# Optimization experiments

Measured on AMD Instinct MI355X. Metric: run time of the kernel, lower is better.

The kernel has to match this reference:

```python
import jax, jax.numpy as jnp
import numpy as np

D = 512    # d_model == EMBED_DIM
H = 8      # nhead
FF = 2048  # dim_feedforward
T, B, S, M = 64, 32, 64, 256
EPS = 1e-5


def setup_inputs() -> dict:
    key = jax.random.key(0)
    ks = iter(jax.random.split(key, 40))
    rn = lambda k, shp, s=0.02: s * jax.random.normal(k, shp, jnp.float32)
    inp = {
        'tgt': jax.random.normal(next(ks), (T, B, D), jnp.float32),
        'memory': jax.random.normal(next(ks), (M, B, D), jnp.float32),
        'semantics': jax.random.normal(next(ks), (B, S, D), jnp.float32),
    }
    for pfx in ('pt', 'sa', 'ca'):  # pre_target, self_attn, cross multihead_attn
        inp[pfx + '_wqkv'] = rn(next(ks), (3 * D, D))
        inp[pfx + '_bqkv'] = jnp.zeros((3 * D,), jnp.float32)
        inp[pfx + '_wo'] = rn(next(ks), (D, D))
        inp[pfx + '_bo'] = jnp.zeros((D,), jnp.float32)
    # relevant_mlp_pre_target: fc0 (2D->D), relu, fc1 (D->D), relu, fc2 (D->1)
    inp['mlp_w0'] = rn(next(ks), (D, 2 * D), float(np.sqrt(2.0 / (2 * D))))
    inp['mlp_b0'] = jnp.zeros((D,), jnp.float32)
    inp['mlp_w1'] = rn(next(ks), (D, D), float(np.sqrt(2.0 / D)))
    inp['mlp_b1'] = jnp.zeros((D,), jnp.float32)
    inp['mlp_w2'] = rn(next(ks), (1, D), float(np.sqrt(2.0 / D)))
    inp['mlp_b2'] = jnp.zeros((1,), jnp.float32)
    inp['ffn_w1'] = rn(next(ks), (FF, D))
    inp['ffn_b1'] = jnp.zeros((FF,), jnp.float32)
    inp['ffn_w2'] = rn(next(ks), (D, FF))
    inp['ffn_b2'] = jnp.zeros((D,), jnp.float32)
    for i in (1, 2, 3):
        inp[f'ln{i}_g'] = jnp.ones((D,), jnp.float32)
        inp[f'ln{i}_b'] = jnp.zeros((D,), jnp.float32)
    return inp


def layernorm(x, g, b):
    mu = jnp.mean(x, -1, keepdims=True)
    var = jnp.var(x, -1, keepdims=True)
    return (x - mu) * jax.lax.rsqrt(var + EPS) * g + b


def mha(q, k, v, wqkv, bqkv, wo, bo):
    # q,k,v: (L, B, D) seq-first, like torch nn.MultiheadAttention
    hd = D // H
    wq, wk, wv = jnp.split(wqkv, 3, axis=0)
    bq, bk, bv = jnp.split(bqkv, 3)
    qh = (q @ wq.T + bq).reshape(q.shape[0], q.shape[1], H, hd)
    kh = (k @ wk.T + bk).reshape(k.shape[0], k.shape[1], H, hd)
    vh = (v @ wv.T + bv).reshape(v.shape[0], v.shape[1], H, hd)
    scale = 1.0 / float(np.sqrt(hd))
    att = jax.nn.softmax(jnp.einsum('qbhd,kbhd->bhqk', qh * scale, kh), axis=-1)
    out = jnp.einsum('bhqk,kbhd->qbhd', att, vh).reshape(q.shape[0], q.shape[1], D)
    return out @ wo.T + bo


def get_relevant_semantic(feats, sem, w0, b0, w1, b1, w2, b2):
    # feats: (B,T,D), sem: (B,S,D). Linear-on-concat == sum of two linears, so we
    # never materialize the (B,T,S,2D) cat tensor; hidden (B,T,S,D) is unavoidable math.
    w0c, w0s = w0[:, :D], w0[:, D:]
    h = (feats @ w0c.T)[:, :, None, :] + (sem @ w0s.T)[:, None, :, :] + b0  # (B,T,S,D)
    h = jax.nn.relu(h)
    h = jax.nn.relu(h @ w1.T + b1)
    scores = h @ w2.T + b2                      # (B,T,S,1)
    a = jax.nn.softmax(scores, axis=2)          # softmax over sem axis
    return jnp.sum(sem[:, None, :, :] * a, axis=2)  # (B,T,D)


def reference(tgt, memory, semantics,
              pt_wqkv, pt_bqkv, pt_wo, pt_bo,
              sa_wqkv, sa_bqkv, sa_wo, sa_bo,
              ca_wqkv, ca_bqkv, ca_wo, ca_bo,
              mlp_w0, mlp_b0, mlp_w1, mlp_b1, mlp_w2, mlp_b2,
              ffn_w1, ffn_b1, ffn_w2, ffn_b2,
              ln1_g, ln1_b, ln2_g, ln2_b, ln3_g, ln3_b):
    # MULTIHEAD_PRE_TARGET branch (eval mode: dropout = identity)
    rel = get_relevant_semantic(jnp.transpose(tgt, (1, 0, 2)), semantics,
                                mlp_w0, mlp_b0, mlp_w1, mlp_b1, mlp_w2, mlp_b2)
    sem_k = jnp.transpose(rel, (1, 0, 2))  # (T,B,D) seq-first key/value
    x = tgt + mha(tgt, sem_k, sem_k, pt_wqkv, pt_bqkv, pt_wo, pt_bo)
    # self attention
    x = layernorm(x + mha(x, x, x, sa_wqkv, sa_bqkv, sa_wo, sa_bo), ln1_g, ln1_b)
    # cross attention over encoder memory
    x = layernorm(x + mha(x, memory, memory, ca_wqkv, ca_bqkv, ca_wo, ca_bo), ln2_g, ln2_b)
    # feed-forward
    ff = jax.nn.relu(x @ ffn_w1.T + ffn_b1) @ ffn_w2.T + ffn_b2
    return layernorm(x + ff, ln3_g, ln3_b)
```

## Files before the change

### kernel.cpp

```cpp
#include <hip/hip_runtime.h>
#include <hip/hip_bf16.h>

#define WS_B 32
#define WS_T 64
#define WS_S 64
#define WS_D 512

typedef __attribute__((ext_vector_type(8))) __bf16 bf16x8;
typedef __attribute__((ext_vector_type(4))) float f32x4;
typedef unsigned short ushort_t;

#define MB(x) ((size_t)(x) << 20)

__device__ __forceinline__ unsigned packpair(float lo, float hi) {
    return ((__float_as_uint(lo) + 0x8000u) >> 16) |
           ((__float_as_uint(hi) + 0x8000u) & 0xffff0000u);
}
__device__ __forceinline__ ushort_t f2bf(float x) {
    return (ushort_t)((__float_as_uint(x) + 0x8000u) >> 16);
}
__device__ __forceinline__ float bf2f(ushort_t u) {
    return __uint_as_float(((unsigned)u) << 16);
}
__device__ __forceinline__ unsigned fuse_word(unsigned f, unsigned s) {
    float lo = __uint_as_float(f << 16) + __uint_as_float(s << 16);
    float hi = __uint_as_float(f & 0xffff0000u) + __uint_as_float(s & 0xffff0000u);
    lo = fmaxf(lo, 0.f);
    hi = fmaxf(hi, 0.f);
    return packpair(lo, hi);
}

struct CvtArgs {
    const float* src[13];
    ushort_t* dst[13];
    int n4[13];
};
__global__ __launch_bounds__(256) void megacvt_kernel(CvtArgs a) {
    const int t = blockIdx.y;
    const int n = a.n4[t];
    const float4* S = (const float4*)a.src[t];
    uint2* D = (uint2*)a.dst[t];
    for (int i = blockIdx.x * 256 + threadIdx.x; i < n; i += gridDim.x * 256) {
        float4 v = S[i];
        uint2 o;
        o.x = packpair(v.x, v.y);
        o.y = packpair(v.z, v.w);
        D[i] = o;
    }
}

__global__ __launch_bounds__(512, 2) void mfma_gemm(
    const ushort_t* __restrict__ A, int lda,
    const ushort_t* __restrict__ W, int ldw,
    const float* __restrict__ bias,
    const float* __restrict__ resid,
    float* __restrict__ C,
    ushort_t* __restrict__ Cb,
    int ldc, int K, int relu)
{
    __shared__ ushort_t As[128 * 32];
    __shared__ ushort_t Bs[256 * 32];
    const int tid = threadIdx.x;
    const int mb = blockIdx.y, nb = blockIdx.x;
    const int w = tid >> 6, lane = tid & 63;
    const int wm = w & 1, wn = w >> 1;
    const int l15 = lane & 15, quad = lane >> 4;
    const int arow = tid >> 2, akc = tid & 3;

    const ushort_t* Ap  = A + (long)(mb * 128 + arow) * lda + akc * 8;
    const ushort_t* Bp0 = W + (long)(nb * 256 + arow) * ldw + akc * 8;
    const ushort_t* Bp1 = Bp0 + (long)128 * ldw;
    ushort_t* Asw  = &As[arow * 32 + akc * 8];
    ushort_t* Bsw0 = &Bs[arow * 32 + akc * 8];
    ushort_t* Bsw1 = Bsw0 + 128 * 32;

    f32x4 acc[4][4];
#pragma unroll
    for (int i = 0; i < 4; ++i)
#pragma unroll
        for (int j = 0; j < 4; ++j) acc[i][j] = (f32x4)0.f;

    for (int k0 = 0; k0 < K; k0 += 32) {
        uint4 av  = *(const uint4*)(Ap + k0);
        uint4 bb0 = *(const uint4*)(Bp0 + k0);
        uint4 bb1 = *(const uint4*)(Bp1 + k0);
        __syncthreads();
        *(uint4*)Asw  = av;
        *(uint4*)Bsw0 = bb0;
        *(uint4*)Bsw1 = bb1;
        __syncthreads();
        bf16x8 af[4], bf[4];
#pragma unroll
        for (int mt = 0; mt < 4; ++mt)
            af[mt] = *(const bf16x8*)&As[(wm * 64 + mt * 16 + l15) * 32 + quad * 8];
#pragma unroll
        for (int nt = 0; nt < 4; ++nt)
            bf[nt] = *(const bf16x8*)&Bs[(wn * 64 + nt * 16 + l15) * 32 + quad * 8];
#pragma unroll
        for (int mt = 0; mt < 4; ++mt)
#pragma unroll
            for (int nt = 0; nt < 4; ++nt)
                acc[mt][nt] = __builtin_amdgcn_mfma_f32_16x16x32_bf16(
                    af[mt], bf[nt], acc[mt][nt], 0, 0, 0);
    }

#pragma unroll
    for (int nt = 0; nt < 4; ++nt) {
        const int col = nb * 256 + wn * 64 + nt * 16 + l15;
        const float bv = bias ? bias[col] : 0.f;
#pragma unroll
        for (int mt = 0; mt < 4; ++mt) {
            const int row0 = mb * 128 + wm * 64 + mt * 16 + quad * 4;
#pragma unroll
            for (int rg = 0; rg < 4; ++rg) {
                float v = acc[mt][nt][rg] + bv;
                if (relu) v = fmaxf(v, 0.f);
                const long off = (long)(row0 + rg) * ldc + col;
                if (resid) v += resid[off];
                if (C) C[off] = v;
                if (Cb) Cb[off] = f2bf(v);
            }
        }
    }
}

__global__ __launch_bounds__(512, 2) void h2score_kernel(
    const ushort_t* __restrict__ Fb,
    const ushort_t* __restrict__ Sb,
    const ushort_t* __restrict__ w1b,
    const float* __restrict__ b1,
    const float* __restrict__ w2,
    float* __restrict__ scores4)
{
    __shared__ ushort_t As[128 * 32];
    __shared__ ushort_t Bs[256 * 32];
    __shared__ float scred[128 * 4];
    const int tid = threadIdx.x;
    const int mb = blockIdx.x, nb = blockIdx.y;
    const int w = tid >> 6, lane = tid & 63;
    const int wm = w & 1, wn = w >> 1;
    const int l15 = lane & 15, quad = lane >> 4;

    const int arow = tid >> 2, akc = tid & 3;
    const int m_g = mb * 128 + arow;
    const int r = m_g >> 6, s = m_g & 63, bidx = r & 31;
    const ushort_t* Fp = Fb + (long)r * 512 + akc * 8;
    const ushort_t* Sp = Sb + (long)(bidx * 64 + s) * 512 + akc * 8;
    const ushort_t* Bp0 = w1b + (long)(nb * 256 + (tid >> 2)) * 512 + (tid & 3) * 8;
    const ushort_t* Bp1 = Bp0 + (long)128 * 512;
    ushort_t* Asw = &As[arow * 32 + akc * 8];
    ushort_t* Bsw0 = &Bs[(tid >> 2) * 32 + (tid & 3) * 8];
    ushort_t* Bsw1 = Bsw0 + 128 * 32;

    f32x4 acc[4][4];
#pragma unroll
    for (int i = 0; i < 4; ++i)
#pragma unroll
        for (int j = 0; j < 4; ++j) acc[i][j] = (f32x4)0.f;

    for (int k0 = 0; k0 < 512; k0 += 32) {
        uint4 fa = *(const uint4*)(Fp + k0);
        uint4 sa = *(const uint4*)(Sp + k0);
        uint4 bb0 = *(const uint4*)(Bp0 + k0);
        uint4 bb1 = *(const uint4*)(Bp1 + k0);
        __syncthreads();
        uint4 o;
        o.x = fuse_word(fa.x, sa.x);
        o.y = fuse_word(fa.y, sa.y);
        o.z = fuse_word(fa.z, sa.z);
        o.w = fuse_word(fa.w, sa.w);
        *(uint4*)Asw = o;
        *(uint4*)Bsw0 = bb0;
        *(uint4*)Bsw1 = bb1;
        __syncthreads();
        bf16x8 af[4], bf[4];
#pragma unroll
        for (int mt = 0; mt < 4; ++mt)
            af[mt] = *(const bf16x8*)&As[(wm * 64 + mt * 16 + l15) * 32 + quad * 8];
#pragma unroll
        for (int nt = 0; nt < 4; ++nt)
            bf[nt] = *(const bf16x8*)&Bs[(wn * 64 + nt * 16 + l15) * 32 + quad * 8];
#pragma unroll
        for (int mt = 0; mt < 4; ++mt)
#pragma unroll
            for (int nt = 0; nt < 4; ++nt)
                acc[mt][nt] = __builtin_amdgcn_mfma_f32_16x16x32_bf16(
                    af[mt], bf[nt], acc[mt][nt], 0, 0, 0);
    }
    __syncthreads();

    float sp[4][4];
#pragma unroll
    for (int mt = 0; mt < 4; ++mt)
#pragma unroll
        for (int rg = 0; rg < 4; ++rg) sp[mt][rg] = 0.f;
#pragma unroll
    for (int nt = 0; nt < 4; ++nt) {
        const int col = nb * 256 + wn * 64 + nt * 16 + l15;
        const float cb = b1[col];
        const float cw = w2[col];
#pragma unroll
        for (int mt = 0; mt < 4; ++mt) {
#pragma unroll
            for (int rg = 0; rg < 4; ++rg)
                sp[mt][rg] += fmaxf(acc[mt][nt][rg] + cb, 0.f) * cw;
        }
    }
#pragma unroll
    for (int mt = 0; mt < 4; ++mt)
#pragma unroll
        for (int rg = 0; rg < 4; ++rg) {
            float v = sp[mt][rg];
            v += __shfl_xor(v, 1);
            v += __shfl_xor(v, 2);
            v += __shfl_xor(v, 4);
            v += __shfl_xor(v, 8);
            if (l15 == 0)
                scred[(wm * 64 + mt * 16 + quad * 4 + rg) * 4 + wn] = v;
        }
    __syncthreads();
    if (tid < 128) {
        float t = scred[tid * 4] + scred[tid * 4 + 1]
                + scred[tid * 4 + 2] + scred[tid * 4 + 3];
        scores4[(long)nb * 131072 + mb * 128 + tid] = t;
    }
}

__global__ __launch_bounds__(256) void softrel_kernel(
    const float* __restrict__ sc4,
    const float* __restrict__ sem,
    ushort_t* __restrict__ rel)
{
    __shared__ float a_s[64];
    const int tid = threadIdx.x;
    const int r = blockIdx.x;
    const int b = r & (WS_B - 1);
    if (tid < 64) {
        float t = sc4[r * 64 + tid] + sc4[131072 + r * 64 + tid];
        float m = t;
#pragma unroll
        for (int off = 32; off > 0; off >>= 1) m = fmaxf(m, __shfl_xor(m, off));
        float e = __expf(t - m);
        float su = e;
#pragma unroll
        for (int off = 32; off > 0; off >>= 1) su += __shfl_xor(su, off);
        a_s[tid] = e / su;
    }
    __syncthreads();
#pragma unroll
    for (int dd = 0; dd < 2; ++dd) {
        const int d = tid + dd * 256;
        float accd = 0.f;
        const float* sp = sem + (long)b * 64 * 512 + d;
        for (int s = 0; s < 64; ++s)
            accd += a_s[s] * sp[s * 512];
        rel[(long)r * 512 + d] = f2bf(accd);
    }
}

__global__ __launch_bounds__(256) void attn2_kernel(
    const ushort_t* __restrict__ Qm, int ldq, int qoff,
    const ushort_t* __restrict__ Km, int ldk, int koff,
    const ushort_t* __restrict__ Vm, int ldv, int voff,
    ushort_t* __restrict__ O,
    int Lk)
{
    __shared__ float sQT[64 * 34];
    __shared__ float sKT[64 * 68];
    __shared__ float sS[32 * 260];
    __shared__ float sredm[8 * 34];
    __shared__ float sreds[8 * 34];
    const int tid = threadIdx.x;
    const int b  = blockIdx.x >> 4;
    const int h  = (blockIdx.x >> 1) & 7;
    const int qt = blockIdx.x & 1;
    const int L8 = Lk >> 3;

    {
        const int q = tid >> 3, c = tid & 7;
        const int qg = qt * 32 + q;
        const ushort_t* pp = Qm + (long)(qg * WS_B + b) * ldq + qoff + h * 64 + c * 8;
        uint4 u = *(const uint4*)pp;
        const ushort_t* us = (const ushort_t*)&u;
#pragma unroll
        for (int i = 0; i < 8; ++i)
            sQT[(c * 8 + i) * 34 + q] = bf2f(us[i]);
    }

    const int k4 = (tid & 15) * 4;
    const int q2 = (tid >> 4) * 2;

    for (int kt = 0; kt < Lk; kt += 64) {
        __syncthreads();
        {
            const int kk = tid >> 3, c = tid & 7;
#pragma unroll
            for (int half = 0; half < 2; ++half) {
                const int kr = kk + half * 32;
                const ushort_t* pp = Km + (long)((kt + kr) * WS_B + b) * ldk + koff + h * 64 + c * 8;
                uint4 u = *(const uint4*)pp;
                const ushort_t* us = (const ushort_t*)&u;
#pragma unroll
                for (int i = 0; i < 8; ++i)
                    sKT[(c * 8 + i) * 68 + kr] = bf2f(us[i]);
            }
        }
        __syncthreads();
        float acc[2][4] = {{0.f, 0.f, 0.f, 0.f}, {0.f, 0.f, 0.f, 0.f}};
        for (int d = 0; d < 64; ++d) {
            const float qa = sQT[d * 34 + q2];
            const float qb = sQT[d * 34 + q2 + 1];
            const float4 kv = *(const float4*)&sKT[d * 68 + k4];
            acc[0][0] += qa * kv.x; acc[0][1] += qa * kv.y;
            acc[0][2] += qa * kv.z; acc[0][3] += qa * kv.w;
            acc[1][0] += qb * kv.x; acc[1][1] += qb * kv.y;
            acc[1][2] += qb * kv.z; acc[1][3] += qb * kv.w;
        }
#pragma unroll
        for (int i = 0; i < 2; ++i) {
            float4 v;
            v.x = acc[i][0] * 0.125f; v.y = acc[i][1] * 0.125f;
            v.z = acc[i][2] * 0.125f; v.w = acc[i][3] * 0.125f;
            *(float4*)&sS[(q2 + i) * 260 + kt + k4] = v;
        }
    }
    __syncthreads();

    {
        const int q = tid & 31, part = tid >> 5;
        const int kb = part * L8;
        float m = -1e30f;
        for (int k = 0; k < L8; ++k) m = fmaxf(m, sS[q * 260 + kb + k]);
        sredm[part * 34 + q] = m;
        __syncthreads();
        float M = sredm[q];
#pragma unroll
        for (int pz = 1; pz < 8; ++pz) M = fmaxf(M, sredm[pz * 34 + q]);
        float su = 0.f;
        for (int k = 0; k < L8; ++k) {
            float e = __expf(sS[q * 260 + kb + k] - M);
            sS[q * 260 + kb + k] = e;
            su += e;
        }
        sreds[part * 34 + q] = su;
    }
    __syncthreads();

    const int d4 = (tid & 15) * 4;
    float o[2][4] = {{0.f, 0.f, 0.f, 0.f}, {0.f, 0.f, 0.f, 0.f}};
    float* sV = sKT;
    for (int kt = 0; kt < Lk; kt += 64) {
        __syncthreads();
        {
            const int kk = tid >> 3, c = tid & 7;
#pragma unroll
            for (int half = 0; half < 2; ++half) {
                const int kr = kk + half * 32;
                const ushort_t* pp = Vm + (long)((kt + kr) * WS_B + b) * ldv + voff + h * 64 + c * 8;
                uint4 u = *(const uint4*)pp;
                const ushort_t* us = (const ushort_t*)&u;
                float4 w0, w1;
                w0.x = bf2f(us[0]); w0.y = bf2f(us[1]);
                w0.z = bf2f(us[2]); w0.w = bf2f(us[3]);
                w1.x = bf2f(us[4]); w1.y = bf2f(us[5]);
                w1.z = bf2f(us[6]); w1.w = bf2f(us[7]);
                *(float4*)&sV[kr * 68 + c * 8] = w0;
                *(float4*)&sV[kr * 68 + c * 8 + 4] = w1;
            }
        }
        __syncthreads();
        for (int k = 0; k < 64; ++k) {
            const float p0 = sS[q2 * 260 + kt + k];
            const float p1 = sS[(q2 + 1) * 260 + kt + k];
            const float4 vv = *(const float4*)&sV[k * 68 + d4];
            o[0][0] += p0 * vv.x; o[0][1] += p0 * vv.y;
            o[0][2] += p0 * vv.z; o[0][3] += p0 * vv.w;
            o[1][0] += p1 * vv.x; o[1][1] += p1 * vv.y;
            o[1][2] += p1 * vv.z; o[1][3] += p1 * vv.w;
        }
    }

#pragma unroll
    for (int i = 0; i < 2; ++i) {
        float su = 0.f;
#pragma unroll
        for (int pz = 0; pz < 8; ++pz) su += sreds[pz * 34 + q2 + i];
        const float inv = 1.f / su;
        const int qg = qt * 32 + q2 + i;
        ushort_t* op = O + (long)(qg * WS_B + b) * 512 + h * 64 + d4;
        uint2 pk;
        pk.x = packpair(o[i][0] * inv, o[i][1] * inv);
        pk.y = packpair(o[i][2] * inv, o[i][3] * inv);
        *(uint2*)op = pk;
    }
}

__global__ __launch_bounds__(256) void ln_kernel(
    const float* __restrict__ X,
    const float* __restrict__ g,
    const float* __restrict__ be,
    float* __restrict__ Y,
    ushort_t* __restrict__ Yb)
{
    const int row = blockIdx.x * 4 + (threadIdx.x >> 6);
    const int lane = threadIdx.x & 63;
    const float4* xp = (const float4*)(X + (long)row * WS_D);
    float4 x0 = xp[lane], x1 = xp[lane + 64];
    float sum = x0.x + x0.y + x0.z + x0.w + x1.x + x1.y + x1.z + x1.w;
    float sq = x0.x * x0.x + x0.y * x0.y + x0.z * x0.z + x0.w * x0.w
             + x1.x * x1.x + x1.y * x1.y + x1.z * x1.z + x1.w * x1.w;
#pragma unroll
    for (int off = 32; off > 0; off >>= 1) {
        sum += __shfl_xor(sum, off);
        sq += __shfl_xor(sq, off);
    }
    const float mu = sum * (1.f / 512.f);
    const float var = sq * (1.f / 512.f) - mu * mu;
    const float rs = rsqrtf(var + 1e-5f);
    const float4* gp = (const float4*)g;
    const float4* bp = (const float4*)be;
    float4 g0 = gp[lane], g1 = gp[lane + 64], b0 = bp[lane], b1 = bp[lane + 64];
    float4 y0, y1;
    y0.x = (x0.x - mu) * rs * g0.x + b0.x;
    y0.y = (x0.y - mu) * rs * g0.y + b0.y;
    y0.z = (x0.z - mu) * rs * g0.z + b0.z;
    y0.w = (x0.w - mu) * rs * g0.w + b0.w;
    y1.x = (x1.x - mu) * rs * g1.x + b1.x;
    y1.y = (x1.y - mu) * rs * g1.y + b1.y;
    y1.z = (x1.z - mu) * rs * g1.z + b1.z;
    y1.w = (x1.w - mu) * rs * g1.w + b1.w;
    float4* yp = (float4*)(Y + (long)row * WS_D);
    yp[lane] = y0; yp[lane + 64] = y1;
    if (Yb) {
        uint2* ybp = (uint2*)(Yb + (long)row * WS_D);
        uint2 p0, p1;
        p0.x = packpair(y0.x, y0.y); p0.y = packpair(y0.z, y0.w);
        p1.x = packpair(y1.x, y1.y); p1.y = packpair(y1.z, y1.w);
        ybp[lane] = p0; ybp[lane + 64] = p1;
    }
}

static inline void mgemm(hipStream_t s, const ushort_t* A, int lda,
                         const ushort_t* W, int ldw, const float* bias,
                         const float* resid, float* C, ushort_t* Cb,
                         int ldc, int M, int N, int K, bool relu)
{
    dim3 g(N / 256, M / 128);
    mfma_gemm<<<g, 512, 0, s>>>(A, lda, W, ldw, bias, resid, C, Cb, ldc, K,
                                relu ? 1 : 0);
}

extern "C" void kernel_launch(void* const* d_in, const int* in_sizes, int n_in,
                              void* d_out, int out_size, void* d_ws, size_t ws_size,
                              hipStream_t stream)
{
    (void)in_sizes; (void)n_in; (void)out_size; (void)ws_size;
    const float* tgt       = (const float*)d_in[0];
    const float* memory    = (const float*)d_in[1];
    const float* semantics = (const float*)d_in[2];
    const float* pt_wqkv   = (const float*)d_in[3];
    const float* pt_bqkv   = (const float*)d_in[4];
    const float* pt_wo     = (const float*)d_in[5];
    const float* pt_bo     = (const float*)d_in[6];
    const float* sa_wqkv   = (const float*)d_in[7];
    const float* sa_bqkv   = (const float*)d_in[8];
    const float* sa_wo     = (const float*)d_in[9];
    const float* sa_bo     = (const float*)d_in[10];
    const float* ca_wqkv   = (const float*)d_in[11];
    const float* ca_bqkv   = (const float*)d_in[12];
    const float* ca_wo     = (const float*)d_in[13];
    const float* ca_bo     = (const float*)d_in[14];
    const float* mlp_w0    = (const float*)d_in[15];
    const float* mlp_b0    = (const float*)d_in[16];
    const float* mlp_w1    = (const float*)d_in[17];
    const float* mlp_b1    = (const float*)d_in[18];
    const float* mlp_w2    = (const float*)d_in[19];
    const float* ffn_w1    = (const float*)d_in[21];
    const float* ffn_b1    = (const float*)d_in[22];
    const float* ffn_w2    = (const float*)d_in[23];
    const float* ffn_b2    = (const float*)d_in[24];
    const float* ln1_g     = (const float*)d_in[25];
    const float* ln1_b     = (const float*)d_in[26];
    const float* ln2_g     = (const float*)d_in[27];
    const float* ln2_b     = (const float*)d_in[28];
    const float* ln3_g     = (const float*)d_in[29];
    const float* ln3_b     = (const float*)d_in[30];

    char* p = (char*)d_ws;
    ushort_t* w0b   = (ushort_t*)(p + 0);
    ushort_t* w1b   = (ushort_t*)(p + MB(1));
    ushort_t* ptwb  = (ushort_t*)(p + 1572864);
    ushort_t* ptob  = (ushort_t*)(p + MB(3));
    ushort_t* sawb  = (ushort_t*)(p + 3670016);
    ushort_t* saob  = (ushort_t*)(p + MB(5));
    ushort_t* cawb  = (ushort_t*)(p + 5767168);
    ushort_t* caob  = (ushort_t*)(p + MB(7));
    ushort_t* f1b   = (ushort_t*)(p + 7864320);
    ushort_t* f2b   = (ushort_t*)(p + 9961472);
    ushort_t* memb  = (ushort_t*)(p + MB(12));
    ushort_t* cakvb = (ushort_t*)(p + MB(20));
    ushort_t* tgtb  = (ushort_t*)(p + MB(36));
    ushort_t* semb  = (ushort_t*)(p + MB(38));
    ushort_t* Fb    = (ushort_t*)(p + MB(40));
    ushort_t* Sb    = (ushort_t*)(p + MB(42));
    float*    scores4 = (float*)(p + MB(44));
    ushort_t* relb  = (ushort_t*)(p + MB(45));
    ushort_t* Ob    = (ushort_t*)(p + MB(47));
    float*    x1f   = (float*)(p + MB(49));
    ushort_t* ptqb  = (ushort_t*)(p + MB(12));
    ushort_t* ptkvb = (ushort_t*)(p + MB(14));
    ushort_t* x1b   = (ushort_t*)(p + MB(18));
    ushort_t* saqkvb= (ushort_t*)(p + MB(38));
    float*    yf    = (float*)(p + MB(12));
    float*    x2f   = (float*)(p + MB(16));
    ushort_t* x2b   = (ushort_t*)(p + MB(36));
    ushort_t* caqb  = (ushort_t*)(p + MB(44));
    float*    x3f   = (float*)(p + MB(40));
    ushort_t* x3b   = (ushort_t*)(p + MB(38));
    ushort_t* hb    = (ushort_t*)(p + MB(20));

    CvtArgs ca;
    ca.src[0]  = tgt;       ca.dst[0]  = tgtb;  ca.n4[0]  = 262144;
    ca.src[1]  = semantics; ca.dst[1]  = semb;  ca.n4[1]  = 262144;
    ca.src[2]  = memory;    ca.dst[2]  = memb;  ca.n4[2]  = 1048576;
    ca.src[3]  = mlp_w0;    ca.dst[3]  = w0b;   ca.n4[3]  = 131072;
    ca.src[4]  = mlp_w1;    ca.dst[4]  = w1b;   ca.n4[4]  = 65536;
    ca.src[5]  = pt_wqkv;   ca.dst[5]  = ptwb;  ca.n4[5]  = 196608;
    ca.src[6]  = pt_wo;     ca.dst[6]  = ptob;  ca.n4[6]  = 65536;
    ca.src[7]  = sa_wqkv;   ca.dst[7]  = sawb;  ca.n4[7]  = 196608;
    ca.src[8]  = sa_wo;     ca.dst[8]  = saob;  ca.n4[8]  = 65536;
    ca.src[9]  = ca_wqkv;   ca.dst[9]  = cawb;  ca.n4[9]  = 196608;
    ca.src[10] = ca_wo;     ca.dst[10] = caob;  ca.n4[10] = 65536;
    ca.src[11] = ffn_w1;    ca.dst[11] = f1b;   ca.n4[11] = 262144;
    ca.src[12] = ffn_w2;    ca.dst[12] = f2b;   ca.n4[12] = 262144;
    megacvt_kernel<<<dim3(1024, 13), 256, 0, stream>>>(ca);

    mgemm(stream, memb, 512, cawb + 512 * 512, 512, ca_bqkv + 512, nullptr,
          nullptr, cakvb, 1024, 8192, 1024, 512, false);

    mgemm(stream, tgtb, 512, w0b, 1024, mlp_b0, nullptr, nullptr, Fb, 512,
          2048, 512, 512, false);
    mgemm(stream, semb, 512, w0b + 512, 1024, nullptr, nullptr, nullptr, Sb, 512,
          2048, 512, 512, false);
    h2score_kernel<<<dim3(1024, 2), 512, 0, stream>>>(Fb, Sb, w1b, mlp_b1,
                                                      mlp_w2, scores4);
    softrel_kernel<<<2048, 256, 0, stream>>>(scores4, semantics, relb);

    mgemm(stream, tgtb, 512, ptwb, 512, pt_bqkv, nullptr, nullptr, ptqb, 512,
          2048, 512, 512, false);
    mgemm(stream, relb, 512, ptwb + 512 * 512, 512, pt_bqkv + 512, nullptr,
          nullptr, ptkvb, 1024, 2048, 1024, 512, false);
    attn2_kernel<<<512, 256, 0, stream>>>(ptqb, 512, 0, ptkvb, 1024, 0,
                                          ptkvb, 1024, 512, Ob, 64);
    mgemm(stream, Ob, 512, ptob, 512, pt_bo, tgt, x1f, x1b, 512,
          2048, 512, 512, false);

    mgemm(stream, x1b, 512, sawb, 512, sa_bqkv, nullptr, nullptr, saqkvb, 1536,
          2048, 1536, 512, false);
    attn2_kernel<<<512, 256, 0, stream>>>(saqkvb, 1536, 0, saqkvb, 1536, 512,
                                          saqkvb, 1536, 1024, Ob, 64);
    mgemm(stream, Ob, 512, saob, 512, sa_bo, x1f, yf, nullptr, 512,
          2048, 512, 512, false);
    ln_kernel<<<512, 256, 0, stream>>>(yf, ln1_g, ln1_b, x2f, x2b);

    mgemm(stream, x2b, 512, cawb, 512, ca_bqkv, nullptr, nullptr, caqb, 512,
          2048, 512, 512, false);
    attn2_kernel<<<512, 256, 0, stream>>>(caqb, 512, 0, cakvb, 1024, 0,
                                          cakvb, 1024, 512, Ob, 256);
    mgemm(stream, Ob, 512, caob, 512, ca_bo, x2f, yf, nullptr, 512,
          2048, 512, 512, false);
    ln_kernel<<<512, 256, 0, stream>>>(yf, ln2_g, ln2_b, x3f, x3b);

    mgemm(stream, x3b, 512, f1b, 512, ffn_b1, nullptr, nullptr, hb, 2048,
          2048, 2048, 512, true);
    mgemm(stream, hb, 2048, f2b, 2048, ffn_b2, x3f, yf, nullptr, 512,
          2048, 512, 2048, false);
    ln_kernel<<<512, 256, 0, stream>>>(yf, ln3_g, ln3_b, (float*)d_out, nullptr);
}
```

Baseline: 615.3 us.

## Batch independent GEMMs into one launch and use direct global-to-LDS loads

Adds a batched GEMM kernel that takes up to four GEMM descriptors and picks one per block from its index. Four independent projections (cross-attention KV, two MLP fc0 halves, pre-target Q) now run in a single launch, cutting launch gaps and filling more CUs. Global-to-shared tile loads now use the global_load_lds builtin instead of loading into registers and storing, and the h2score kernel also prefetches its fused A operand one step ahead. ptq moves to a new buffer so it is not overwritten, at the cost of more workspace and per-block descriptor selection overhead.

```diff
diff --git a/kernel.cpp b/kernel.cpp
--- a/kernel.cpp
+++ b/kernel.cpp
@@ -28,6 +28,11 @@
     lo = fmaxf(lo, 0.f);
     hi = fmaxf(hi, 0.f);
     return packpair(lo, hi);
+}
+__device__ __forceinline__ void gl2lds16(const void* g, void* l) {
+    __builtin_amdgcn_global_load_lds(
+        (const __attribute__((address_space(1))) void*)g,
+        (__attribute__((address_space(3))) void*)l, 16, 0, 0);
 }
 
 struct CvtArgs {
@@ -49,30 +54,43 @@
     }
 }
 
-__global__ __launch_bounds__(512, 2) void mfma_gemm(
-    const ushort_t* __restrict__ A, int lda,
-    const ushort_t* __restrict__ W, int ldw,
-    const float* __restrict__ bias,
-    const float* __restrict__ resid,
-    float* __restrict__ C,
-    ushort_t* __restrict__ Cb,
-    int ldc, int K, int relu)
-{
+struct GemmDesc {
+    const ushort_t* A;
+    const ushort_t* W;
+    const float* bias;
+    const float* resid;
+    float* C;
+    ushort_t* Cb;
+    int lda, ldw, ldc, K, relu, nbx, blkStart;
+};
+struct GemmBatch {
+    GemmDesc d[4];
+    int nd;
+};
+
+__global__ __launch_bounds__(512, 2) void mfma_gemm_b(GemmBatch bt) {
     __shared__ ushort_t As[128 * 32];
     __shared__ ushort_t Bs[256 * 32];
+    int di = 0;
+#pragma unroll
+    for (int i = 1; i < 4; ++i)
+        if (i < bt.nd && (int)blockIdx.x >= bt.d[i].blkStart) di = i;
+    const GemmDesc g = bt.d[di];
+    const int local = blockIdx.x - g.blkStart;
+    const int mb = local / g.nbx;
+    const int nb = local - mb * g.nbx;
+
     const int tid = threadIdx.x;
-    const int mb = blockIdx.y, nb = blockIdx.x;
     const int w = tid >> 6, lane = tid & 63;
     const int wm = w & 1, wn = w >> 1;
     const int l15 = lane & 15, quad = lane >> 4;
-    const int arow = tid >> 2, akc = tid & 3;
-
-    const ushort_t* Ap  = A + (long)(mb * 128 + arow) * lda + akc * 8;
-    const ushort_t* Bp0 = W + (long)(nb * 256 + arow) * ldw + akc * 8;
-    const ushort_t* Bp1 = Bp0 + (long)128 * ldw;
-    ushort_t* Asw  = &As[arow * 32 + akc * 8];
-    ushort_t* Bsw0 = &Bs[arow * 32 + akc * 8];
-    ushort_t* Bsw1 = Bsw0 + 128 * 32;
+
+    const ushort_t* Ap  = g.A + (long)(mb * 128 + (tid >> 2)) * g.lda + (tid & 3) * 8;
+    const ushort_t* Bp0 = g.W + (long)(nb * 256 + (tid >> 2)) * g.ldw + (tid & 3) * 8;
+    const ushort_t* Bp1 = Bp0 + (long)128 * g.ldw;
+    ushort_t* AsD  = As + w * 512;
+    ushort_t* BsD0 = Bs + w * 512;
+    ushort_t* BsD1 = Bs + 4096 + w * 512;
 
     f32x4 acc[4][4];
 #pragma unroll
@@ -80,14 +98,11 @@
 #pragma unroll
         for (int j = 0; j < 4; ++j) acc[i][j] = (f32x4)0.f;
 
-    for (int k0 = 0; k0 < K; k0 += 32) {
-        uint4 av  = *(const uint4*)(Ap + k0);
-        uint4 bb0 = *(const uint4*)(Bp0 + k0);
-        uint4 bb1 = *(const uint4*)(Bp1 + k0);
-        __syncthreads();
-        *(uint4*)Asw  = av;
-        *(uint4*)Bsw0 = bb0;
-        *(uint4*)Bsw1 = bb1;
+    for (int k0 = 0; k0 < g.K; k0 += 32) {
+        __syncthreads();
+        gl2lds16(Ap + k0, AsD);
+        gl2lds16(Bp0 + k0, BsD0);
+        gl2lds16(Bp1 + k0, BsD1);
         __syncthreads();
         bf16x8 af[4], bf[4];
 #pragma unroll
@@ -107,18 +122,18 @@
 #pragma unroll
     for (int nt = 0; nt < 4; ++nt) {
         const int col = nb * 256 + wn * 64 + nt * 16 + l15;
-        const float bv = bias ? bias[col] : 0.f;
+        const float bv = g.bias ? g.bias[col] : 0.f;
 #pragma unroll
         for (int mt = 0; mt < 4; ++mt) {
             const int row0 = mb * 128 + wm * 64 + mt * 16 + quad * 4;
 #pragma unroll
             for (int rg = 0; rg < 4; ++rg) {
                 float v = acc[mt][nt][rg] + bv;
-                if (relu) v = fmaxf(v, 0.f);
-                const long off = (long)(row0 + rg) * ldc + col;
-                if (resid) v += resid[off];
-                if (C) C[off] = v;
-                if (Cb) Cb[off] = f2bf(v);
+                if (g.relu) v = fmaxf(v, 0.f);
+                const long off = (long)(row0 + rg) * g.ldc + col;
+                if (g.resid) v += g.resid[off];
+                if (g.C) g.C[off] = v;
+                if (g.Cb) g.Cb[off] = f2bf(v);
             }
         }
     }
@@ -149,8 +164,8 @@
     const ushort_t* Bp0 = w1b + (long)(nb * 256 + (tid >> 2)) * 512 + (tid & 3) * 8;
     const ushort_t* Bp1 = Bp0 + (long)128 * 512;
     ushort_t* Asw = &As[arow * 32 + akc * 8];
-    ushort_t* Bsw0 = &Bs[(tid >> 2) * 32 + (tid & 3) * 8];
-    ushort_t* Bsw1 = Bsw0 + 128 * 32;
+    ushort_t* BsD0 = Bs + w * 512;
+    ushort_t* BsD1 = Bs + 4096 + w * 512;
 
     f32x4 acc[4][4];
 #pragma unroll
@@ -158,20 +173,22 @@
 #pragma unroll
         for (int j = 0; j < 4; ++j) acc[i][j] = (f32x4)0.f;
 
+    uint4 fa = *(const uint4*)(Fp);
+    uint4 sa = *(const uint4*)(Sp);
     for (int k0 = 0; k0 < 512; k0 += 32) {
-        uint4 fa = *(const uint4*)(Fp + k0);
-        uint4 sa = *(const uint4*)(Sp + k0);
-        uint4 bb0 = *(const uint4*)(Bp0 + k0);
-        uint4 bb1 = *(const uint4*)(Bp1 + k0);
-        __syncthreads();
+        __syncthreads();
+        gl2lds16(Bp0 + k0, BsD0);
+        gl2lds16(Bp1 + k0, BsD1);
         uint4 o;
         o.x = fuse_word(fa.x, sa.x);
         o.y = fuse_word(fa.y, sa.y);
         o.z = fuse_word(fa.z, sa.z);
         o.w = fuse_word(fa.w, sa.w);
         *(uint4*)Asw = o;
-        *(uint4*)Bsw0 = bb0;
-        *(uint4*)Bsw1 = bb1;
+        if (k0 + 32 < 512) {
+            fa = *(const uint4*)(Fp + k0 + 32);
+            sa = *(const uint4*)(Sp + k0 + 32);
+        }
         __syncthreads();
         bf16x8 af[4], bf[4];
 #pragma unroll
@@ -440,14 +457,28 @@
     }
 }
 
+static inline GemmDesc mkdesc(const ushort_t* A, int lda, const ushort_t* W, int ldw,
+                              const float* bias, const float* resid, float* C,
+                              ushort_t* Cb, int ldc, int N, int K, int relu,
+                              int blkStart)
+{
+    GemmDesc d;
+    d.A = A; d.W = W; d.bias = bias; d.resid = resid; d.C = C; d.Cb = Cb;
+    d.lda = lda; d.ldw = ldw; d.ldc = ldc; d.K = K; d.relu = relu;
+    d.nbx = N / 256;
+    d.blkStart = blkStart;
+    return d;
+}
 static inline void mgemm(hipStream_t s, const ushort_t* A, int lda,
                          const ushort_t* W, int ldw, const float* bias,
                          const float* resid, float* C, ushort_t* Cb,
                          int ldc, int M, int N, int K, bool relu)
 {
-    dim3 g(N / 256, M / 128);
-    mfma_gemm<<<g, 512, 0, s>>>(A, lda, W, ldw, bias, resid, C, Cb, ldc, K,
-                                relu ? 1 : 0);
+    GemmBatch bt;
+    bt.nd = 1;
+    bt.d[0] = mkdesc(A, lda, W, ldw, bias, resid, C, Cb, ldc, N, K, relu ? 1 : 0, 0);
+    bt.d[1] = bt.d[0]; bt.d[2] = bt.d[0]; bt.d[3] = bt.d[0];
+    mfma_gemm_b<<<(M / 128) * (N / 256), 512, 0, s>>>(bt);
 }
 
 extern "C" void kernel_launch(void* const* d_in, const int* in_sizes, int n_in,
@@ -507,7 +538,7 @@
     ushort_t* relb  = (ushort_t*)(p + MB(45));
     ushort_t* Ob    = (ushort_t*)(p + MB(47));
     float*    x1f   = (float*)(p + MB(49));
-    ushort_t* ptqb  = (ushort_t*)(p + MB(12));
+    ushort_t* ptqb  = (ushort_t*)(p + MB(53));
     ushort_t* ptkvb = (ushort_t*)(p + MB(14));
     ushort_t* x1b   = (ushort_t*)(p + MB(18));
     ushort_t* saqkvb= (ushort_t*)(p + MB(38));
@@ -535,19 +566,24 @@
     ca.src[12] = ffn_w2;    ca.dst[12] = f2b;   ca.n4[12] = 262144;
     megacvt_kernel<<<dim3(1024, 13), 256, 0, stream>>>(ca);
 
-    mgemm(stream, memb, 512, cawb + 512 * 512, 512, ca_bqkv + 512, nullptr,
-          nullptr, cakvb, 1024, 8192, 1024, 512, false);
-
-    mgemm(stream, tgtb, 512, w0b, 1024, mlp_b0, nullptr, nullptr, Fb, 512,
-          2048, 512, 512, false);
-    mgemm(stream, semb, 512, w0b + 512, 1024, nullptr, nullptr, nullptr, Sb, 512,
-          2048, 512, 512, false);
+    {
+        GemmBatch bt;
+        bt.nd = 4;
+        bt.d[0] = mkdesc(memb, 512, cawb + 512 * 512, 512, ca_bqkv + 512, nullptr,
+                         nullptr, cakvb, 1024, 1024, 512, 0, 0);
+        bt.d[1] = mkdesc(tgtb, 512, w0b, 1024, mlp_b0, nullptr,
+                         nullptr, Fb, 512, 512, 512, 0, 256);
+        bt.d[2] = mkdesc(semb, 512, w0b + 512, 1024, nullptr, nullptr,
+                         nullptr, Sb, 512, 512, 512, 0, 288);
+        bt.d[3] = mkdesc(tgtb, 512, ptwb, 512, pt_bqkv, nullptr,
+                         nullptr, ptqb, 512, 512, 512, 0, 320);
+        mfma_gemm_b<<<352, 512, 0, stream>>>(bt);
+    }
+
     h2score_kernel<<<dim3(1024, 2), 512, 0, stream>>>(Fb, Sb, w1b, mlp_b1,
                                                       mlp_w2, scores4);
     softrel_kernel<<<2048, 256, 0, stream>>>(scores4, semantics, relb);
 
-    mgemm(stream, tgtb, 512, ptwb, 512, pt_bqkv, nullptr, nullptr, ptqb, 512,
-          2048, 512, 512, false);
     mgemm(stream, relb, 512, ptwb + 512 * 512, 512, pt_bqkv + 512, nullptr,
           nullptr, ptkvb, 1024, 2048, 1024, 512, false);
     attn2_kernel<<<512, 256, 0, stream>>>(ptqb, 512, 0, ptkvb, 1024, 0,
```

Measured after the change: 612.5 us. About the same (-0.5%).
